# Kernel optimization log

Measured on AMD Instinct MI355X. Metric: run time of the kernel, lower is better.

Reference implementation:

```python
import jax, jax.numpy as jnp
import numpy as np

B, S, H, NH = 4, 2048, 1024, 16
HD = H // NH
EPS = 1e-12


def setup_inputs() -> dict:
    key = jax.random.key(0)
    ks = jax.random.split(key, 12)
    sc = 0.02
    return {
        "query": jax.random.normal(ks[0], (B, S, H), dtype=jnp.float32),
        "attention_mask": jnp.zeros((B, 1, 1, S), dtype=jnp.float32),
        "Wq": jax.random.normal(ks[1], (H, H), dtype=jnp.float32) * sc,
        "bq": jnp.zeros((H,), dtype=jnp.float32),
        "Wk": jax.random.normal(ks[2], (H, H), dtype=jnp.float32) * sc,
        "bk": jnp.zeros((H,), dtype=jnp.float32),
        "Wv": jax.random.normal(ks[3], (H, H), dtype=jnp.float32) * sc,
        "bv": jnp.zeros((H,), dtype=jnp.float32),
        "Wd": jax.random.normal(ks[4], (H, H), dtype=jnp.float32) * sc,
        "bd": jnp.zeros((H,), dtype=jnp.float32),
        "ln_gamma": jnp.ones((H,), dtype=jnp.float32),
        "ln_beta": jnp.zeros((H,), dtype=jnp.float32),
    }


def reference(query, attention_mask, Wq, bq, Wk, bk, Wv, bv, Wd, bd, ln_gamma, ln_beta):
    # QKV projections: [B,S,H] -> [B,S,NH,HD]
    q = (query @ Wq + bq).reshape(B, S, NH, HD)
    k = (query @ Wk + bk).reshape(B, S, NH, HD)
    v = (query @ Wv + bv).reshape(B, S, NH, HD)
    # scores: [B,NH,S,S]
    scores = jnp.einsum("bqhd,bkhd->bhqk", q, k) / jnp.sqrt(jnp.float32(HD))
    scores = scores + attention_mask
    probs = jax.nn.softmax(scores, axis=-1)  # attn_dropout p=0 (eval)
    ctx = jnp.einsum("bhqk,bkhd->bqhd", probs, v).reshape(B, S, H)
    hidden = ctx @ Wd + bd  # out_dropout p=0 (eval)
    # pre-LN residual path: LN(hidden) + query
    mu = jnp.mean(hidden, axis=-1, keepdims=True)
    var = jnp.mean(jnp.square(hidden - mu), axis=-1, keepdims=True)
    hidden = (hidden - mu) * jax.lax.rsqrt(var + EPS) * ln_gamma + ln_beta
    return hidden + query
```

## Files before the change

kernel.cpp:

```cpp
#include <hip/hip_runtime.h>
#include <stdint.h>

#define Bn 4
#define Sn 2048
#define Hn 1024
#define NHn 16
#define Mn 8192

typedef unsigned short bf_t;
typedef __attribute__((ext_vector_type(8))) short s16x8;
typedef __attribute__((ext_vector_type(4))) short s16x4;
typedef __attribute__((ext_vector_type(8))) unsigned short u16x8;
typedef __attribute__((ext_vector_type(4))) unsigned short u16x4;
typedef __attribute__((ext_vector_type(4))) float f32x4;
typedef __attribute__((ext_vector_type(4))) unsigned int u32x4;
typedef __attribute__((ext_vector_type(2))) unsigned int u32x2;

__device__ __forceinline__ bf_t f2bf(float f) {
  unsigned int u = __float_as_uint(f);
  u += 0x7fffu + ((u >> 16) & 1u);
  return (bf_t)(u >> 16);
}

__device__ __forceinline__ unsigned pk2(float lo, float hi) {
  return __builtin_amdgcn_perm(__float_as_uint(hi), __float_as_uint(lo), 0x07060302u);
}
__device__ __forceinline__ s16x4 pack4(float a0, float a1, float a2, float a3) {
  u32x2 t;
  t[0] = pk2(a0, a1);
  t[1] = pk2(a2, a3);
  return __builtin_bit_cast(s16x4, t);
}

#define MFMA16K16(a, b, c) __builtin_amdgcn_mfma_f32_16x16x16bf16_1k(a, b, c, 0, 0, 0)

#define GLOAD16(gp, lp) __builtin_amdgcn_global_load_lds(              \
    (__attribute__((address_space(1))) void*)(gp),                     \
    (__attribute__((address_space(3))) void*)(lp), 16, 0, 0)

__global__ __launch_bounds__(256)
void cvt_bf16(const float* __restrict__ x, bf_t* __restrict__ y) {
  size_t i = ((size_t)blockIdx.x * 256 + threadIdx.x) * 4;
  const f32x4 v = *(const f32x4*)(x + i);
  u16x4 o;
  o[0] = f2bf(v[0]); o[1] = f2bf(v[1]); o[2] = f2bf(v[2]); o[3] = f2bf(v[3]);
  *(u16x4*)(y + i) = o;
}

__global__ __launch_bounds__(256)
void wtrans(const float* __restrict__ W, bf_t* __restrict__ Wt) {
  __shared__ float tile[32][33];
  const int tx = threadIdx.x;
  const int ty = threadIdx.y;
  const int n0 = blockIdx.x * 32, k0 = blockIdx.y * 32;
#pragma unroll
  for (int i = 0; i < 4; i++)
    tile[ty + i * 8][tx] = W[(size_t)(k0 + ty + i * 8) * Hn + n0 + tx];
  __syncthreads();
#pragma unroll
  for (int i = 0; i < 4; i++) {
    const int nn = ty + i * 8, kk = tx;
    Wt[(size_t)(n0 + nn) * Hn + k0 + kk] = f2bf(tile[kk][nn]);
  }
}

__global__ __launch_bounds__(256)
void gemm_bt(const bf_t* __restrict__ A, const bf_t* __restrict__ Bt,
             const float* __restrict__ b0, const float* __restrict__ b1,
             const float* __restrict__ b2, void* __restrict__ outp,
             int N, int K, int out_bf16)
{
  __shared__ bf_t As[128 * 32];
  __shared__ bf_t Bs[128 * 32];
  const int tid = threadIdx.x;
  const int wave = tid >> 6, lane = tid & 63;
  const int l15 = lane & 15, quad = lane >> 4;
  const int bm = blockIdx.y * 128, bn = blockIdx.x * 128;
  const int wm = (wave >> 1) * 64, wn = (wave & 1) * 64;
  const int srow = tid >> 2;
  const int scol = (tid & 3) * 8;

  const bf_t* Ag = A + (size_t)(bm + srow) * K + scol;
  const bf_t* Bg = Bt + (size_t)(bn + srow) * K + scol;

  f32x4 acc[4][4] = {};

  for (int k0 = 0; k0 < K; k0 += 32) {
    __syncthreads();
    GLOAD16(Ag + k0, As + tid * 8);
    GLOAD16(Ag + (size_t)64 * K + k0, As + 2048 + tid * 8);
    GLOAD16(Bg + k0, Bs + tid * 8);
    GLOAD16(Bg + (size_t)64 * K + k0, Bs + 2048 + tid * 8);
    __syncthreads();
    s16x8 af[4], bfr[4];
#pragma unroll
    for (int mi = 0; mi < 4; mi++)
      af[mi] = *(const s16x8*)&As[(wm + mi * 16 + l15) * 32 + quad * 8];
#pragma unroll
    for (int ni = 0; ni < 4; ni++)
      bfr[ni] = *(const s16x8*)&Bs[(wn + ni * 16 + l15) * 32 + quad * 8];
#pragma unroll
    for (int mi = 0; mi < 4; mi++)
#pragma unroll
      for (int ni = 0; ni < 4; ni++)
        acc[mi][ni] = __builtin_amdgcn_mfma_f32_16x16x32_bf16(af[mi], bfr[ni], acc[mi][ni], 0, 0, 0);
  }

#pragma unroll
  for (int ni = 0; ni < 4; ni++) {
    const int gn = bn + wn + ni * 16 + l15;
    const float* bp = (gn < 1024) ? b0 : ((gn < 2048) ? b1 : b2);
    const float bias = bp[gn & 1023];
#pragma unroll
    for (int mi = 0; mi < 4; mi++) {
#pragma unroll
      for (int r = 0; r < 4; r++) {
        const int gm = bm + wm + mi * 16 + quad * 4 + r;
        const float v = acc[mi][ni][r] + bias;
        if (out_bf16) ((bf_t*)outp)[(size_t)gm * N + gn] = f2bf(v);
        else          ((float*)outp)[(size_t)gm * N + gn] = v;
      }
    }
  }
}

__global__ __launch_bounds__(256)
void kswz(const bf_t* __restrict__ qkv, bf_t* __restrict__ Kf) {
  __shared__ bf_t KT[64 * 80];
  const int t = threadIdx.x;
  const int bh = blockIdx.y, b = bh >> 4, h = bh & 15;
  const int t64 = blockIdx.x * 64;
#pragma unroll
  for (int i = 0; i < 2; i++) {
    const int c = t + i * 256;
    const int row = c >> 3, col8 = (c & 7) * 8;
    const u16x8 v = *(const u16x8*)(qkv + (size_t)(b * Sn + t64 + row) * 3072 + 1024 + h * 64 + col8);
    *(u16x8*)&KT[row * 80 + col8] = v;
  }
  __syncthreads();
  bf_t* dst0 = Kf + ((size_t)(bh * 32 + blockIdx.x) * 8) * 512;
#pragma unroll
  for (int i = 0; i < 2; i++) {
    const int p = t + i * 256;
    const int frag = p >> 6, lane = p & 63;
    const int ks = frag >> 1, half = frag & 1;
    const int l15 = lane & 15, quad = lane >> 4;
    const u16x8 v = *(const u16x8*)&KT[(ks * 16 + l15) * 80 + half * 32 + quad * 8];
    *(u16x8*)(dst0 + (size_t)frag * 512 + lane * 8) = v;
  }
}

__global__ __launch_bounds__(256)
void vswz(const bf_t* __restrict__ qkv, bf_t* __restrict__ Vf) {
  __shared__ unsigned int P32[64 * 33];
  const int t = threadIdx.x;
  const int bh = blockIdx.y, b = bh >> 4, h = bh & 15;
  const int k0 = blockIdx.x * 64;
  {
    const int kp = t >> 3;
    const int d0 = (t & 7) * 8;
    const bf_t* p0 = qkv + (size_t)(b * Sn + k0 + 2 * kp) * 3072 + 2048 + h * 64 + d0;
    const u16x8 r0 = *(const u16x8*)p0;
    const u16x8 r1 = *(const u16x8*)(p0 + 3072);
#pragma unroll
    for (int j = 0; j < 8; j++)
      P32[(d0 + j) * 33 + kp] = (unsigned)r0[j] | ((unsigned)r1[j] << 16);
  }
  __syncthreads();
  bf_t* dst0 = Vf + ((size_t)(bh * 32 + blockIdx.x) * 8) * 512;
#pragma unroll
  for (int i = 0; i < 2; i++) {
    const int p = t + i * 256;
    const int fp = p >> 6, lane = p & 63;
    const int dvblk = fp >> 1, kpair = fp & 1;
    const int l15 = lane & 15, quad = (lane >> 4) & 3;
    const int d = dvblk * 16 + l15;
    const int c = kpair * 16 + quad * 2;
    u32x4 w;
    w[0] = P32[d * 33 + c];
    w[1] = P32[d * 33 + c + 1];
    w[2] = P32[d * 33 + c + 8];
    w[3] = P32[d * 33 + c + 9];
    *(u32x4*)(dst0 + (size_t)fp * 512 + lane * 8) = w;
  }
}

__global__ __launch_bounds__(256)
void attn(const bf_t* __restrict__ qkv, const bf_t* __restrict__ Kf,
          const bf_t* __restrict__ Vf, const float* __restrict__ mask,
          bf_t* __restrict__ ctx)
{
  __shared__ bf_t Ks[2][4096];
  __shared__ bf_t Vs[2][4096];

  const int tid = threadIdx.x;
  const int wave = tid >> 6, lane = tid & 63;
  const int l15 = lane & 15, quad = lane >> 4;
  const int idx = blockIdx.x;
  const int bh = idx & 63, b = bh >> 4, h = bh & 15;
  const int q0 = (idx >> 6) * 128;

  s16x8 aq[2][2];
#pragma unroll
  for (int qf = 0; qf < 2; qf++) {
    const bf_t* qp = qkv + (size_t)(b * Sn + q0 + wave * 32 + qf * 16 + l15) * 3072 + h * 64;
    aq[qf][0] = *(const s16x8*)(qp + quad * 8);
    aq[qf][1] = *(const s16x8*)(qp + 32 + quad * 8);
  }

  float l_i[2] = {0.f, 0.f};
  f32x4 o[2][4] = {};

  const bf_t* kb = Kf + (size_t)bh * 32 * 4096;
  const bf_t* vb = Vf + (size_t)bh * 32 * 4096;
  const float* mrow = mask + (size_t)b * Sn;

  const float C1 = 0.125f * 1.44269504f;
  const float LOG2E = 1.44269504f;

#pragma unroll
  for (int c = 0; c < 2; c++) {
    GLOAD16(kb + c * 2048 + tid * 8, Ks[0] + c * 2048 + tid * 8);
    GLOAD16(vb + c * 2048 + tid * 8, Vs[0] + c * 2048 + tid * 8);
  }

  for (int it = 0; it < 32; ++it) {
    const int cur = it & 1;
    __syncthreads();
    if (it < 31) {
      const bf_t* kn = kb + (size_t)(it + 1) * 4096;
      const bf_t* vn = vb + (size_t)(it + 1) * 4096;
#pragma unroll
      for (int c = 0; c < 2; c++) {
        GLOAD16(kn + c * 2048 + tid * 8, Ks[cur ^ 1] + c * 2048 + tid * 8);
        GLOAD16(vn + c * 2048 + tid * 8, Vs[cur ^ 1] + c * 2048 + tid * 8);
      }
    }

    s16x4 pb[2][4];
#pragma unroll
    for (int e = 0; e < 4; e++) {
      const s16x8 k0f = *(const s16x8*)&Ks[cur][(e * 2 + 0) * 512 + lane * 8];
      const s16x8 k1f = *(const s16x8*)&Ks[cur][(e * 2 + 1) * 512 + lane * 8];
      const f32x4 mk = *(const f32x4*)(mrow + it * 64 + e * 16 + quad * 4);
      f32x4 mk2;
#pragma unroll
      for (int r = 0; r < 4; r++) mk2[r] = mk[r] * LOG2E;
#pragma unroll
      for (int qf = 0; qf < 2; qf++) {
        f32x4 acc = {};
        acc = __builtin_amdgcn_mfma_f32_16x16x32_bf16(k0f, aq[qf][0], acc, 0, 0, 0);
        acc = __builtin_amdgcn_mfma_f32_16x16x32_bf16(k1f, aq[qf][1], acc, 0, 0, 0);
        const float p0 = __builtin_exp2f(fmaf(acc[0], C1, mk2[0]));
        const float p1 = __builtin_exp2f(fmaf(acc[1], C1, mk2[1]));
        const float p2 = __builtin_exp2f(fmaf(acc[2], C1, mk2[2]));
        const float p3 = __builtin_exp2f(fmaf(acc[3], C1, mk2[3]));
        l_i[qf] += (p0 + p1) + (p2 + p3);
        pb[qf][e] = pack4(p0, p1, p2, p3);
      }
    }

#pragma unroll
    for (int kpair = 0; kpair < 2; kpair++)
#pragma unroll
      for (int dvblk = 0; dvblk < 4; dvblk++) {
        const s16x8 vv = *(const s16x8*)&Vs[cur][(dvblk * 2 + kpair) * 512 + lane * 8];
        const s16x4 vlo = {vv[0], vv[1], vv[2], vv[3]};
        const s16x4 vhi = {vv[4], vv[5], vv[6], vv[7]};
#pragma unroll
        for (int qf = 0; qf < 2; qf++) {
          o[qf][dvblk] = MFMA16K16(vlo, pb[qf][kpair * 2 + 0], o[qf][dvblk]);
          o[qf][dvblk] = MFMA16K16(vhi, pb[qf][kpair * 2 + 1], o[qf][dvblk]);
        }
      }
  }

#pragma unroll
  for (int qf = 0; qf < 2; qf++) {
    float l = l_i[qf];
    l += __shfl_xor(l, 16);
    l += __shfl_xor(l, 32);
    const float inv = 1.f / l;
    const size_t row = (size_t)(b * Sn + q0 + wave * 32 + qf * 16 + l15);
#pragma unroll
    for (int dvblk = 0; dvblk < 4; dvblk++) {
      u16x4 ov;
#pragma unroll
      for (int r = 0; r < 4; r++) ov[r] = f2bf(o[qf][dvblk][r] * inv);
      *(u16x4*)&ctx[row * Hn + h * 64 + dvblk * 16 + quad * 4] = ov;
    }
  }
}

__global__ __launch_bounds__(256)
void ln_res(const float* __restrict__ hid, const float* __restrict__ query,
            const float* __restrict__ gamma, const float* __restrict__ beta,
            float* __restrict__ out)
{
  const int row = blockIdx.x, t = threadIdx.x;
  const f32x4 h = *(const f32x4*)(hid + (size_t)row * Hn + t * 4);
  float s = h[0] + h[1] + h[2] + h[3];
  float ss = h[0]*h[0] + h[1]*h[1] + h[2]*h[2] + h[3]*h[3];
#pragma unroll
  for (int m = 32; m; m >>= 1) { s += __shfl_xor(s, m); ss += __shfl_xor(ss, m); }
  __shared__ float red[8];
  if ((t & 63) == 0) { red[t >> 6] = s; red[4 + (t >> 6)] = ss; }
  __syncthreads();
  s = red[0] + red[1] + red[2] + red[3];
  ss = red[4] + red[5] + red[6] + red[7];
  const float mu = s * (1.f / Hn);
  const float rs = rsqrtf(ss * (1.f / Hn) - mu * mu + 1e-12f);
  const f32x4 q = *(const f32x4*)(query + (size_t)row * Hn + t * 4);
  const f32x4 g = *(const f32x4*)(gamma + t * 4);
  const f32x4 be = *(const f32x4*)(beta + t * 4);
  f32x4 o;
#pragma unroll
  for (int j = 0; j < 4; j++) o[j] = (h[j] - mu) * rs * g[j] + be[j] + q[j];
  *(f32x4*)(out + (size_t)row * Hn + t * 4) = o;
}

extern "C" void kernel_launch(void* const* d_in, const int* in_sizes, int n_in,
                              void* d_out, int out_size, void* d_ws, size_t ws_size,
                              hipStream_t stream) {
  const float* query = (const float*)d_in[0];
  const float* mask  = (const float*)d_in[1];
  const float* Wq = (const float*)d_in[2];
  const float* bq = (const float*)d_in[3];
  const float* Wk = (const float*)d_in[4];
  const float* bk = (const float*)d_in[5];
  const float* Wv = (const float*)d_in[6];
  const float* bv = (const float*)d_in[7];
  const float* Wd = (const float*)d_in[8];
  const float* bd = (const float*)d_in[9];
  const float* gamma = (const float*)d_in[10];
  const float* beta  = (const float*)d_in[11];

  char* w = (char*)d_ws;
  bf_t* Xb  = (bf_t*)w;  w += (size_t)Mn * Hn * 2;
  bf_t* Wt  = (bf_t*)w;  w += (size_t)3 * Hn * Hn * 2;
  bf_t* Wdt = (bf_t*)w;  w += (size_t)Hn * Hn * 2;
  bf_t* QKV = (bf_t*)w;  w += (size_t)Mn * 3 * Hn * 2;
  bf_t* Vf  = (bf_t*)w;  w += (size_t)64 * 32 * 4096 * 2;
  bf_t* Ctx = (bf_t*)w;  w += (size_t)Mn * Hn * 2;
  bf_t* Kf  = (bf_t*)w;
  float* Hid = (float*)w;

  cvt_bf16<<<Mn * Hn / 1024, 256, 0, stream>>>(query, Xb);
  dim3 tb(32, 8);
  wtrans<<<dim3(32, 32), tb, 0, stream>>>(Wq, Wt);
  wtrans<<<dim3(32, 32), tb, 0, stream>>>(Wk, Wt + (size_t)Hn * Hn);
  wtrans<<<dim3(32, 32), tb, 0, stream>>>(Wv, Wt + (size_t)2 * Hn * Hn);
  wtrans<<<dim3(32, 32), tb, 0, stream>>>(Wd, Wdt);
  gemm_bt<<<dim3(24, 64), 256, 0, stream>>>(Xb, Wt, bq, bk, bv, QKV, 3072, 1024, 1);
  kswz<<<dim3(32, 64), 256, 0, stream>>>(QKV, Kf);
  vswz<<<dim3(32, 64), 256, 0, stream>>>(QKV, Vf);
  attn<<<1024, 256, 0, stream>>>(QKV, Kf, Vf, mask, Ctx);
  gemm_bt<<<dim3(8, 64), 256, 0, stream>>>(Ctx, Wdt, bd, bd, bd, Hid, 1024, 1024, 0);
  ln_res<<<Mn, 256, 0, stream>>>(Hid, query, gamma, beta, (float*)d_out);
}
```

Baseline: 379.2 us.

## Double-buffer GEMM loads, merge prep kernels, precompute scaled mask, MFMA row sums

The GEMM now double-buffers its LDS tiles so the next K-slice's global-to-LDS loads are issued before the current slice is computed, and it drops one barrier per iteration. It also sets a minimum of 3 blocks per CU in launch bounds. The four weight-transpose launches become one 3D launch, and the K and V swizzle kernels are merged into one launch that also writes a log2e-scaled copy of the mask. Attention reads that pre-scaled mask and computes the softmax row sums with an MFMA against a vector of bf16 ones instead of scalar adds and shuffles. The risks are doubled LDS per GEMM block, extra register pressure, and row sums taken from bf16-rounded probabilities.

```diff
diff --git a/kernel.cpp b/kernel.cpp
--- a/kernel.cpp
+++ b/kernel.cpp
@@ -48,8 +48,13 @@
 }
 
 __global__ __launch_bounds__(256)
-void wtrans(const float* __restrict__ W, bf_t* __restrict__ Wt) {
+void wtrans4(const float* __restrict__ Wq, const float* __restrict__ Wk,
+             const float* __restrict__ Wv, const float* __restrict__ Wd,
+             bf_t* __restrict__ Wt, bf_t* __restrict__ Wdt) {
   __shared__ float tile[32][33];
+  const int z = blockIdx.z;
+  const float* W = (z == 0) ? Wq : (z == 1) ? Wk : (z == 2) ? Wv : Wd;
+  bf_t* dst = (z < 3) ? Wt + (size_t)z * Hn * Hn : Wdt;
   const int tx = threadIdx.x;
   const int ty = threadIdx.y;
   const int n0 = blockIdx.x * 32, k0 = blockIdx.y * 32;
@@ -60,18 +65,18 @@
 #pragma unroll
   for (int i = 0; i < 4; i++) {
     const int nn = ty + i * 8, kk = tx;
-    Wt[(size_t)(n0 + nn) * Hn + k0 + kk] = f2bf(tile[kk][nn]);
-  }
-}
-
-__global__ __launch_bounds__(256)
+    dst[(size_t)(n0 + nn) * Hn + k0 + kk] = f2bf(tile[kk][nn]);
+  }
+}
+
+__global__ __launch_bounds__(256, 3)
 void gemm_bt(const bf_t* __restrict__ A, const bf_t* __restrict__ Bt,
              const float* __restrict__ b0, const float* __restrict__ b1,
              const float* __restrict__ b2, void* __restrict__ outp,
              int N, int K, int out_bf16)
 {
-  __shared__ bf_t As[128 * 32];
-  __shared__ bf_t Bs[128 * 32];
+  __shared__ bf_t As[2][4096];
+  __shared__ bf_t Bs[2][4096];
   const int tid = threadIdx.x;
   const int wave = tid >> 6, lane = tid & 63;
   const int l15 = lane & 15, quad = lane >> 4;
@@ -85,20 +90,29 @@
 
   f32x4 acc[4][4] = {};
 
-  for (int k0 = 0; k0 < K; k0 += 32) {
+  GLOAD16(Ag, As[0] + tid * 8);
+  GLOAD16(Ag + (size_t)64 * K, As[0] + 2048 + tid * 8);
+  GLOAD16(Bg, Bs[0] + tid * 8);
+  GLOAD16(Bg + (size_t)64 * K, Bs[0] + 2048 + tid * 8);
+
+  const int nIter = K >> 5;
+  for (int i = 0; i < nIter; i++) {
+    const int cur = i & 1;
     __syncthreads();
-    GLOAD16(Ag + k0, As + tid * 8);
-    GLOAD16(Ag + (size_t)64 * K + k0, As + 2048 + tid * 8);
-    GLOAD16(Bg + k0, Bs + tid * 8);
-    GLOAD16(Bg + (size_t)64 * K + k0, Bs + 2048 + tid * 8);
-    __syncthreads();
+    if (i + 1 < nIter) {
+      const int k0 = (i + 1) * 32;
+      GLOAD16(Ag + k0, As[cur ^ 1] + tid * 8);
+      GLOAD16(Ag + (size_t)64 * K + k0, As[cur ^ 1] + 2048 + tid * 8);
+      GLOAD16(Bg + k0, Bs[cur ^ 1] + tid * 8);
+      GLOAD16(Bg + (size_t)64 * K + k0, Bs[cur ^ 1] + 2048 + tid * 8);
+    }
     s16x8 af[4], bfr[4];
 #pragma unroll
     for (int mi = 0; mi < 4; mi++)
-      af[mi] = *(const s16x8*)&As[(wm + mi * 16 + l15) * 32 + quad * 8];
+      af[mi] = *(const s16x8*)&As[cur][(wm + mi * 16 + l15) * 32 + quad * 8];
 #pragma unroll
     for (int ni = 0; ni < 4; ni++)
-      bfr[ni] = *(const s16x8*)&Bs[(wn + ni * 16 + l15) * 32 + quad * 8];
+      bfr[ni] = *(const s16x8*)&Bs[cur][(wn + ni * 16 + l15) * 32 + quad * 8];
 #pragma unroll
     for (int mi = 0; mi < 4; mi++)
 #pragma unroll
@@ -125,69 +139,71 @@
 }
 
 __global__ __launch_bounds__(256)
-void kswz(const bf_t* __restrict__ qkv, bf_t* __restrict__ Kf) {
-  __shared__ bf_t KT[64 * 80];
-  const int t = threadIdx.x;
-  const int bh = blockIdx.y, b = bh >> 4, h = bh & 15;
-  const int t64 = blockIdx.x * 64;
-#pragma unroll
-  for (int i = 0; i < 2; i++) {
-    const int c = t + i * 256;
-    const int row = c >> 3, col8 = (c & 7) * 8;
-    const u16x8 v = *(const u16x8*)(qkv + (size_t)(b * Sn + t64 + row) * 3072 + 1024 + h * 64 + col8);
-    *(u16x8*)&KT[row * 80 + col8] = v;
-  }
-  __syncthreads();
-  bf_t* dst0 = Kf + ((size_t)(bh * 32 + blockIdx.x) * 8) * 512;
-#pragma unroll
-  for (int i = 0; i < 2; i++) {
-    const int p = t + i * 256;
-    const int frag = p >> 6, lane = p & 63;
-    const int ks = frag >> 1, half = frag & 1;
-    const int l15 = lane & 15, quad = lane >> 4;
-    const u16x8 v = *(const u16x8*)&KT[(ks * 16 + l15) * 80 + half * 32 + quad * 8];
-    *(u16x8*)(dst0 + (size_t)frag * 512 + lane * 8) = v;
-  }
-}
-
-__global__ __launch_bounds__(256)
-void vswz(const bf_t* __restrict__ qkv, bf_t* __restrict__ Vf) {
-  __shared__ unsigned int P32[64 * 33];
+void kvswz(const bf_t* __restrict__ qkv, bf_t* __restrict__ Kf,
+           bf_t* __restrict__ Vf, const float* __restrict__ mask,
+           float* __restrict__ mask2) {
+  __shared__ u32x4 smbuf[640];
   const int t = threadIdx.x;
   const int bh = blockIdx.y, b = bh >> 4, h = bh & 15;
   const int k0 = blockIdx.x * 64;
-  {
-    const int kp = t >> 3;
-    const int d0 = (t & 7) * 8;
-    const bf_t* p0 = qkv + (size_t)(b * Sn + k0 + 2 * kp) * 3072 + 2048 + h * 64 + d0;
-    const u16x8 r0 = *(const u16x8*)p0;
-    const u16x8 r1 = *(const u16x8*)(p0 + 3072);
-#pragma unroll
-    for (int j = 0; j < 8; j++)
-      P32[(d0 + j) * 33 + kp] = (unsigned)r0[j] | ((unsigned)r1[j] << 16);
-  }
-  __syncthreads();
-  bf_t* dst0 = Vf + ((size_t)(bh * 32 + blockIdx.x) * 8) * 512;
-#pragma unroll
-  for (int i = 0; i < 2; i++) {
-    const int p = t + i * 256;
-    const int fp = p >> 6, lane = p & 63;
-    const int dvblk = fp >> 1, kpair = fp & 1;
-    const int l15 = lane & 15, quad = (lane >> 4) & 3;
-    const int d = dvblk * 16 + l15;
-    const int c = kpair * 16 + quad * 2;
-    u32x4 w;
-    w[0] = P32[d * 33 + c];
-    w[1] = P32[d * 33 + c + 1];
-    w[2] = P32[d * 33 + c + 8];
-    w[3] = P32[d * 33 + c + 9];
-    *(u32x4*)(dst0 + (size_t)fp * 512 + lane * 8) = w;
+
+  if (blockIdx.z == 0) {
+    bf_t* KT = (bf_t*)smbuf;
+#pragma unroll
+    for (int i = 0; i < 2; i++) {
+      const int c = t + i * 256;
+      const int row = c >> 3, col8 = (c & 7) * 8;
+      const u16x8 v = *(const u16x8*)(qkv + (size_t)(b * Sn + k0 + row) * 3072 + 1024 + h * 64 + col8);
+      *(u16x8*)&KT[row * 80 + col8] = v;
+    }
+    __syncthreads();
+    bf_t* dst0 = Kf + ((size_t)(bh * 32 + blockIdx.x) * 8) * 512;
+#pragma unroll
+    for (int i = 0; i < 2; i++) {
+      const int p = t + i * 256;
+      const int frag = p >> 6, lane = p & 63;
+      const int ks = frag >> 1, half = frag & 1;
+      const int l15 = lane & 15, quad = lane >> 4;
+      const u16x8 v = *(const u16x8*)&KT[(ks * 16 + l15) * 80 + half * 32 + quad * 8];
+      *(u16x8*)(dst0 + (size_t)frag * 512 + lane * 8) = v;
+    }
+  } else {
+    unsigned int* P32 = (unsigned int*)smbuf;
+    {
+      const int kp = t >> 3;
+      const int d0 = (t & 7) * 8;
+      const bf_t* p0 = qkv + (size_t)(b * Sn + k0 + 2 * kp) * 3072 + 2048 + h * 64 + d0;
+      const u16x8 r0 = *(const u16x8*)p0;
+      const u16x8 r1 = *(const u16x8*)(p0 + 3072);
+#pragma unroll
+      for (int j = 0; j < 8; j++)
+        P32[(d0 + j) * 33 + kp] = (unsigned)r0[j] | ((unsigned)r1[j] << 16);
+    }
+    if (h == 0 && t < 64)
+      mask2[b * Sn + k0 + t] = mask[b * Sn + k0 + t] * 1.44269504f;
+    __syncthreads();
+    bf_t* dst0 = Vf + ((size_t)(bh * 32 + blockIdx.x) * 8) * 512;
+#pragma unroll
+    for (int i = 0; i < 2; i++) {
+      const int p = t + i * 256;
+      const int fp = p >> 6, lane = p & 63;
+      const int dvblk = fp >> 1, kpair = fp & 1;
+      const int l15 = lane & 15, quad = (lane >> 4) & 3;
+      const int d = dvblk * 16 + l15;
+      const int c = kpair * 16 + quad * 2;
+      u32x4 w;
+      w[0] = P32[d * 33 + c];
+      w[1] = P32[d * 33 + c + 1];
+      w[2] = P32[d * 33 + c + 8];
+      w[3] = P32[d * 33 + c + 9];
+      *(u32x4*)(dst0 + (size_t)fp * 512 + lane * 8) = w;
+    }
   }
 }
 
 __global__ __launch_bounds__(256)
 void attn(const bf_t* __restrict__ qkv, const bf_t* __restrict__ Kf,
-          const bf_t* __restrict__ Vf, const float* __restrict__ mask,
+          const bf_t* __restrict__ Vf, const float* __restrict__ mask2,
           bf_t* __restrict__ ctx)
 {
   __shared__ bf_t Ks[2][4096];
@@ -208,15 +224,15 @@
     aq[qf][1] = *(const s16x8*)(qp + 32 + quad * 8);
   }
 
-  float l_i[2] = {0.f, 0.f};
+  f32x4 lacc[2] = {};
   f32x4 o[2][4] = {};
+  const s16x4 ONES = {16256, 16256, 16256, 16256};
 
   const bf_t* kb = Kf + (size_t)bh * 32 * 4096;
   const bf_t* vb = Vf + (size_t)bh * 32 * 4096;
-  const float* mrow = mask + (size_t)b * Sn;
+  const float* m2row = mask2 + (size_t)b * Sn;
 
   const float C1 = 0.125f * 1.44269504f;
-  const float LOG2E = 1.44269504f;
 
 #pragma unroll
   for (int c = 0; c < 2; c++) {
@@ -242,10 +258,7 @@
     for (int e = 0; e < 4; e++) {
       const s16x8 k0f = *(const s16x8*)&Ks[cur][(e * 2 + 0) * 512 + lane * 8];
       const s16x8 k1f = *(const s16x8*)&Ks[cur][(e * 2 + 1) * 512 + lane * 8];
-      const f32x4 mk = *(const f32x4*)(mrow + it * 64 + e * 16 + quad * 4);
-      f32x4 mk2;
-#pragma unroll
-      for (int r = 0; r < 4; r++) mk2[r] = mk[r] * LOG2E;
+      const f32x4 mk2 = *(const f32x4*)(m2row + it * 64 + e * 16 + quad * 4);
 #pragma unroll
       for (int qf = 0; qf < 2; qf++) {
         f32x4 acc = {};
@@ -255,8 +268,8 @@
         const float p1 = __builtin_exp2f(fmaf(acc[1], C1, mk2[1]));
         const float p2 = __builtin_exp2f(fmaf(acc[2], C1, mk2[2]));
         const float p3 = __builtin_exp2f(fmaf(acc[3], C1, mk2[3]));
-        l_i[qf] += (p0 + p1) + (p2 + p3);
         pb[qf][e] = pack4(p0, p1, p2, p3);
+        lacc[qf] = MFMA16K16(ONES, pb[qf][e], lacc[qf]);
       }
     }
 
@@ -277,10 +290,7 @@
 
 #pragma unroll
   for (int qf = 0; qf < 2; qf++) {
-    float l = l_i[qf];
-    l += __shfl_xor(l, 16);
-    l += __shfl_xor(l, 32);
-    const float inv = 1.f / l;
+    const float inv = 1.f / lacc[qf][0];
     const size_t row = (size_t)(b * Sn + q0 + wave * 32 + qf * 16 + l15);
 #pragma unroll
     for (int dvblk = 0; dvblk < 4; dvblk++) {
@@ -343,18 +353,14 @@
   bf_t* Vf  = (bf_t*)w;  w += (size_t)64 * 32 * 4096 * 2;
   bf_t* Ctx = (bf_t*)w;  w += (size_t)Mn * Hn * 2;
   bf_t* Kf  = (bf_t*)w;
-  float* Hid = (float*)w;
+  float* Hid = (float*)w;  w += (size_t)Mn * Hn * 4;
+  float* Mask2 = (float*)w;
 
   cvt_bf16<<<Mn * Hn / 1024, 256, 0, stream>>>(query, Xb);
-  dim3 tb(32, 8);
-  wtrans<<<dim3(32, 32), tb, 0, stream>>>(Wq, Wt);
-  wtrans<<<dim3(32, 32), tb, 0, stream>>>(Wk, Wt + (size_t)Hn * Hn);
-  wtrans<<<dim3(32, 32), tb, 0, stream>>>(Wv, Wt + (size_t)2 * Hn * Hn);
-  wtrans<<<dim3(32, 32), tb, 0, stream>>>(Wd, Wdt);
+  wtrans4<<<dim3(32, 32, 4), dim3(32, 8), 0, stream>>>(Wq, Wk, Wv, Wd, Wt, Wdt);
   gemm_bt<<<dim3(24, 64), 256, 0, stream>>>(Xb, Wt, bq, bk, bv, QKV, 3072, 1024, 1);
-  kswz<<<dim3(32, 64), 256, 0, stream>>>(QKV, Kf);
-  vswz<<<dim3(32, 64), 256, 0, stream>>>(QKV, Vf);
-  attn<<<1024, 256, 0, stream>>>(QKV, Kf, Vf, mask, Ctx);
+  kvswz<<<dim3(32, 64, 2), 256, 0, stream>>>(QKV, Kf, Vf, mask, Mask2);
+  attn<<<1024, 256, 0, stream>>>(QKV, Kf, Vf, Mask2, Ctx);
   gemm_bt<<<dim3(8, 64), 256, 0, stream>>>(Ctx, Wdt, bd, bd, bd, Hid, 1024, 1024, 0);
   ln_res<<<Mn, 256, 0, stream>>>(Hid, query, gamma, beta, (float*)d_out);
 }
```

Result: faster. 362.7 us (-4.3%).
